# Optimization experiments

Measured on AMD Instinct MI355X. Metric: run time of the kernel, lower is better.

The kernel has to match this reference:

```python
import jax, jax.numpy as jnp
import numpy as np

B, T, D, H, O = 128, 1024, 256, 512, 256


def setup_inputs() -> dict:
    key = jax.random.key(0)
    ks = jax.random.split(key, 7)
    s = lambda k, shape, fan: jax.random.normal(k, shape, dtype=jnp.float32) / np.sqrt(fan)
    return {
        "x": jax.random.normal(ks[0], (B, T, D), dtype=jnp.float32),
        "W_ih": s(ks[1], (4 * H, D), D),
        "W_hh": s(ks[2], (4 * H, H), H),
        "b_ih": jnp.zeros((4 * H,), dtype=jnp.float32),
        "b_hh": jnp.zeros((4 * H,), dtype=jnp.float32),
        "W_out": s(ks[5], (O, H), H),
        "b_out": jnp.zeros((O,), dtype=jnp.float32),
    }


def reference(x, W_ih, W_hh, b_ih, b_hh, W_out, b_out):
    Bsz = x.shape[0]
    Hd = W_hh.shape[1]
    # Precompute input projections for all timesteps: [B, T, 4H]
    x_proj = jnp.einsum("btd,gd->btg", x, W_ih) + b_ih + b_hh

    def step(carry, xp_t):
        h, c = carry
        gates = xp_t + h @ W_hh.T  # [B, 4H]
        i, f, g, o = jnp.split(gates, 4, axis=-1)
        i = jax.nn.sigmoid(i)
        f = jax.nn.sigmoid(f)
        g = jnp.tanh(g)
        o = jax.nn.sigmoid(o)
        c = f * c + i * g
        h = o * jnp.tanh(c)
        return (h, c), None

    h0 = jnp.zeros((Bsz, Hd), dtype=x.dtype)
    c0 = jnp.zeros((Bsz, Hd), dtype=x.dtype)
    (h_T, _), _ = jax.lax.scan(step, (h0, c0), jnp.swapaxes(x_proj, 0, 1))
    return h_T @ W_out.T + b_out
```

## Files before the change

kernel.cpp:

```cpp
#include <hip/hip_runtime.h>

#define Bsz 128
#define Tlen 1024
#define Din 256
#define Hdim 512

#define NBG 8
#define NCG 16

typedef __attribute__((ext_vector_type(8))) short short8;
typedef __attribute__((ext_vector_type(4))) float f32x4;
typedef __attribute__((ext_vector_type(4))) unsigned short ushort4_;
typedef __attribute__((ext_vector_type(4))) unsigned int uint4v;

#define HBT_BYTES ((size_t)2 * NBG * 16 * Hdim * 4)
#define HT_OFF ((size_t)524288)

__device__ inline unsigned short f2bf(float f) {
    unsigned int u = __builtin_bit_cast(unsigned int, f);
    unsigned int lsb = (u >> 16) & 1u;
    u += 0x7fffu + lsb;
    return (unsigned short)(u >> 16);
}
__device__ inline float bf2f(unsigned short u) {
    unsigned int v = ((unsigned int)u) << 16;
    return __builtin_bit_cast(float, v);
}
__device__ inline float sigm_f(float x) { return 1.f / (1.f + __expf(-x)); }
__device__ inline float tanh_f(float x) { return 1.f - 2.f / (__expf(2.f * x) + 1.f); }

__device__ __forceinline__ void conv_x_to_lds(const float4* xv, int tid,
                                              unsigned char* xh, unsigned char* xl) {
#pragma unroll
    for (int i = 0; i < 2; i++) {
        int cidx = tid + i * 512;
        int row = cidx >> 6;
        int c4 = cidx & 63;
        float vv[4] = {xv[i].x, xv[i].y, xv[i].z, xv[i].w};
        ushort4_ vh, vl;
#pragma unroll
        for (int e = 0; e < 4; e++) {
            unsigned short hi = f2bf(vv[e]);
            vh[e] = hi;
            vl[e] = f2bf(vv[e] - bf2f(hi));
        }
        int a = ((row << 9) + (c4 << 3)) ^ ((row & 7) << 4);
        *(ushort4_*)(xh + a) = vh;
        *(ushort4_*)(xl + a) = vl;
    }
}

__device__ __forceinline__ bool chunk_ok(uint4v v, unsigned want) {
    unsigned m =
        ((v[0] ^ want) | (v[1] ^ want) | (v[2] ^ want) | (v[3] ^ want)) & 0xFFFFu;
    return m == 0;
}
__device__ __forceinline__ void chunk_to_lds(uint4v v, int c, unsigned char* h_lds) {
    int row = c >> 7;
    unsigned lo = (v[0] >> 16) | (v[1] & 0xFFFF0000u);
    unsigned hi = (v[2] >> 16) | (v[3] & 0xFFFF0000u);
    int a = ((row << 10) + ((c & 127) << 3)) ^ ((row & 7) << 4);
    *(unsigned long long*)(h_lds + a) =
        (unsigned long long)lo | ((unsigned long long)hi << 32);
}

__global__ __launch_bounds__(512, 1) void lstm_persist(
    const float* __restrict__ x, const float* __restrict__ Wih,
    const float* __restrict__ Whh, const float* __restrict__ bih,
    const float* __restrict__ bhh, unsigned int* __restrict__ hbt,
    float* __restrict__ hT) {
    __shared__ unsigned char h_lds[16 * 1024];
    __shared__ unsigned char xh_lds[2 * 8192];
    __shared__ unsigned char xl_lds[2 * 8192];
    __shared__ float gates_w[8][16 * 17];

    const int tid = threadIdx.x;
    const int bid = blockIdx.x;
    const int bg = bid & 7;
    const int cg = bid >> 3;
    const int lane = tid & 63;
    const int w = tid >> 6;
    const int n15 = lane & 15;
    const int k8 = lane >> 4;
    const int grow = bg * 16;
    const int gc = n15 & 3;
    const int gsel = n15 >> 2;
    const int myb = k8 * 4 + gsel;
    const int mycol = cg * 32 + w * 4 + gc;

    const int R = (n15 >> 2) * Hdim + mycol;
    short8 whh[16], wihh[8], wihl[8];
    {
        const float* wr = Whh + (size_t)R * Hdim;
#pragma unroll
        for (int kc = 0; kc < 16; kc++) {
            const float* p = wr + kc * 32 + k8 * 8;
            short8 f;
#pragma unroll
            for (int e = 0; e < 8; e++) f[e] = (short)f2bf(p[e]);
            whh[kc] = f;
        }
        const float* wr2 = Wih + (size_t)R * Din;
#pragma unroll
        for (int kc = 0; kc < 8; kc++) {
            const float* p = wr2 + kc * 32 + k8 * 8;
            short8 fh, fl;
#pragma unroll
            for (int e = 0; e < 8; e++) {
                float v = p[e];
                unsigned short hi = f2bf(v);
                fh[e] = (short)hi;
                fl[e] = (short)f2bf(v - bf2f(hi));
            }
            wihh[kc] = fh;
            wihl[kc] = fl;
        }
    }
    float bias4[4];
#pragma unroll
    for (int g = 0; g < 4; g++) bias4[g] = bih[g * Hdim + mycol] + bhh[g * Hdim + mycol];

    float4 xr[2];
    {
        const float* xb = x + (size_t)grow * (Tlen * Din);
#pragma unroll
        for (int i = 0; i < 2; i++) {
            int cidx = tid + i * 512;
            int row = cidx >> 6;
            int c4 = cidx & 63;
            xr[i] = *(const float4*)(xb + (size_t)row * (Tlen * Din) + c4 * 4);
        }
        conv_x_to_lds(xr, tid, xh_lds, xl_lds);
#pragma unroll
        for (int i = 0; i < 2; i++) {
            int cidx = tid + i * 512;
            int row = cidx >> 6;
            int c4 = cidx & 63;
            xr[i] = *(const float4*)(xb + (size_t)row * (Tlen * Din) + Din + c4 * 4);
        }
    }
    __syncthreads();

    float c_reg = 0.f, h_last = 0.f;

    for (int t = 0; t < Tlen; ++t) {
        if (t + 1 < Tlen)
            conv_x_to_lds(xr, tid, xh_lds + ((t + 1) & 1) * 8192,
                          xl_lds + ((t + 1) & 1) * 8192);

        const unsigned int* hb = hbt + ((size_t)(t & 1) * NBG + bg) * 8192;
        const unsigned int* p0 = hb + (size_t)tid * 4;
        const unsigned int* p1 = hb + (size_t)(tid + 512) * 4;
        const unsigned int* p2 = hb + (size_t)(tid + 1024) * 4;
        const unsigned int* p3 = hb + (size_t)(tid + 1536) * 4;
        uint4v r0, r1, r2, r3;
        if (t > 0) {
            asm volatile(
                "global_load_dwordx4 %0, %4, off sc0 sc1\n\t"
                "global_load_dwordx4 %1, %5, off sc0 sc1\n\t"
                "global_load_dwordx4 %2, %6, off sc0 sc1\n\t"
                "global_load_dwordx4 %3, %7, off sc0 sc1"
                : "=&v"(r0), "=&v"(r1), "=&v"(r2), "=&v"(r3)
                : "v"(p0), "v"(p1), "v"(p2), "v"(p3)
                : "memory");
        }

        unsigned char* xh = xh_lds + (t & 1) * 8192;
        unsigned char* xl = xl_lds + (t & 1) * 8192;
        f32x4 acc0 = {0.f, 0.f, 0.f, 0.f}, acc1 = {0.f, 0.f, 0.f, 0.f};
#pragma unroll
        for (int kc = 0; kc < 8; kc++) {
            int a = ((n15 << 9) + (kc << 6) + (k8 << 4)) ^ ((n15 & 7) << 4);
            short8 xhv = *(const short8*)(xh + a);
            short8 xlv = *(const short8*)(xl + a);
            acc0 = __builtin_amdgcn_mfma_f32_16x16x32_bf16(xhv, wihh[kc], acc0, 0, 0, 0);
            acc1 = __builtin_amdgcn_mfma_f32_16x16x32_bf16(xlv, wihh[kc], acc1, 0, 0, 0);
            if (kc & 1)
                acc1 = __builtin_amdgcn_mfma_f32_16x16x32_bf16(xhv, wihl[kc], acc1, 0, 0, 0);
            else
                acc0 = __builtin_amdgcn_mfma_f32_16x16x32_bf16(xhv, wihl[kc], acc0, 0, 0, 0);
        }

        if (t > 0) {
            const unsigned want = (unsigned)t;
            asm volatile("s_waitcnt vmcnt(0)" ::: "memory");
            __builtin_amdgcn_sched_barrier(0);
            unsigned need = 0;
            if (chunk_ok(r0, want)) chunk_to_lds(r0, tid, h_lds); else need |= 1u;
            if (chunk_ok(r1, want)) chunk_to_lds(r1, tid + 512, h_lds); else need |= 2u;
            if (chunk_ok(r2, want)) chunk_to_lds(r2, tid + 1024, h_lds); else need |= 4u;
            if (chunk_ok(r3, want)) chunk_to_lds(r3, tid + 1536, h_lds); else need |= 8u;
            int rounds = 0;
            while (need && ++rounds < (1 << 14)) {
                if (rounds > 6) __builtin_amdgcn_s_sleep(2);
                if (need & 1u)
                    asm volatile("global_load_dwordx4 %0, %1, off sc0 sc1"
                                 : "=&v"(r0) : "v"(p0) : "memory");
                if (need & 2u)
                    asm volatile("global_load_dwordx4 %0, %1, off sc0 sc1"
                                 : "=&v"(r1) : "v"(p1) : "memory");
                if (need & 4u)
                    asm volatile("global_load_dwordx4 %0, %1, off sc0 sc1"
                                 : "=&v"(r2) : "v"(p2) : "memory");
                if (need & 8u)
                    asm volatile("global_load_dwordx4 %0, %1, off sc0 sc1"
                                 : "=&v"(r3) : "v"(p3) : "memory");
                asm volatile("s_waitcnt vmcnt(0)" ::: "memory");
                __builtin_amdgcn_sched_barrier(0);
                if ((need & 1u) && chunk_ok(r0, want)) {
                    chunk_to_lds(r0, tid, h_lds);
                    need &= ~1u;
                }
                if ((need & 2u) && chunk_ok(r1, want)) {
                    chunk_to_lds(r1, tid + 512, h_lds);
                    need &= ~2u;
                }
                if ((need & 4u) && chunk_ok(r2, want)) {
                    chunk_to_lds(r2, tid + 1024, h_lds);
                    need &= ~4u;
                }
                if ((need & 8u) && chunk_ok(r3, want)) {
                    chunk_to_lds(r3, tid + 1536, h_lds);
                    need &= ~8u;
                }
            }
        } else {
#pragma unroll
            for (int i = 0; i < 4; i++) {
                int c = tid + i * 512;
                int row = c >> 7;
                int a = ((row << 10) + ((c & 127) << 3)) ^ ((row & 7) << 4);
                *(unsigned long long*)(h_lds + a) = 0ULL;
            }
        }
        __syncthreads();

#pragma unroll
        for (int kc = 0; kc < 16; kc++) {
            short8 a = *(const short8*)(h_lds + (((n15 << 10) + (kc << 6) + (k8 << 4)) ^
                                                ((n15 & 7) << 4)));
            if (kc & 1)
                acc1 = __builtin_amdgcn_mfma_f32_16x16x32_bf16(a, whh[kc], acc1, 0, 0, 0);
            else
                acc0 = __builtin_amdgcn_mfma_f32_16x16x32_bf16(a, whh[kc], acc0, 0, 0, 0);
        }

        if (t + 2 < Tlen) {
            const float* xb = x + (size_t)grow * (Tlen * Din) + (size_t)(t + 2) * Din;
#pragma unroll
            for (int i = 0; i < 2; i++) {
                int cidx = tid + i * 512;
                int row = cidx >> 6;
                int c4 = cidx & 63;
                xr[i] = *(const float4*)(xb + (size_t)row * (Tlen * Din) + c4 * 4);
            }
        }

        float* gt = gates_w[w];
#pragma unroll
        for (int j2 = 0; j2 < 4; j2++) gt[(k8 * 4 + j2) * 17 + n15] = acc0[j2] + acc1[j2];
        {
            float pre[4];
#pragma unroll
            for (int g = 0; g < 4; g++) pre[g] = gt[myb * 17 + g * 4 + gc] + bias4[g];
            float ig = sigm_f(pre[0]);
            float fg = sigm_f(pre[1]);
            float gg = tanh_f(pre[2]);
            float og = sigm_f(pre[3]);
            c_reg = fg * c_reg + ig * gg;
            h_last = og * tanh_f(c_reg);
            unsigned int word = ((unsigned int)f2bf(h_last) << 16) | (unsigned)(t + 1);
            unsigned int* dst = hbt + ((size_t)((t + 1) & 1) * NBG + bg) * 8192 +
                                (size_t)myb * Hdim + mycol;
            __hip_atomic_store(dst, word, __ATOMIC_RELAXED, __HIP_MEMORY_SCOPE_AGENT);
        }
        __syncthreads();
    }

    hT[(size_t)(grow + myb) * Hdim + mycol] = h_last;
}

__global__ __launch_bounds__(256) void out_proj(const float* __restrict__ hT,
                                                const float* __restrict__ Wout,
                                                const float* __restrict__ bout,
                                                float* __restrict__ out) {
    __shared__ float h_s[16 * 512];
    __shared__ float w_s[64 * 69];
    const int tid = threadIdx.x;
    const int bt = blockIdx.x >> 2;
    const int ot = blockIdx.x & 3;
#pragma unroll
    for (int i = 0; i < 8; i++) {
        int cidx = tid + i * 256;
        int row = cidx >> 7;
        int c4 = cidx & 127;
        *(float4*)(&h_s[row * 512 + c4 * 4]) =
            *(const float4*)(hT + (size_t)(bt * 16 + row) * 512 + c4 * 4);
    }
    const int o = tid & 63;
    const int bq = tid >> 6;
    float acc[4] = {0.f, 0.f, 0.f, 0.f};
    for (int kc = 0; kc < 8; kc++) {
        __syncthreads();
#pragma unroll
        for (int i = 0; i < 4; i++) {
            int cidx = tid + i * 256;
            int row = cidx >> 4;
            int c4 = cidx & 15;
            float4 v = *(const float4*)(Wout + (size_t)(ot * 64 + row) * 512 + kc * 64 +
                                        c4 * 4);
            float* dst = &w_s[row * 69 + c4 * 4];
            dst[0] = v.x;
            dst[1] = v.y;
            dst[2] = v.z;
            dst[3] = v.w;
        }
        __syncthreads();
#pragma unroll 16
        for (int k = 0; k < 64; k++) {
            float wv = w_s[o * 69 + k];
#pragma unroll
            for (int bi = 0; bi < 4; bi++)
                acc[bi] += h_s[(bq * 4 + bi) * 512 + kc * 64 + k] * wv;
        }
    }
    float bo = bout[ot * 64 + o];
#pragma unroll
    for (int bi = 0; bi < 4; bi++)
        out[(size_t)(bt * 16 + bq * 4 + bi) * 256 + ot * 64 + o] = acc[bi] + bo;
}

extern "C" void kernel_launch(void* const* d_in, const int* in_sizes, int n_in,
                              void* d_out, int out_size, void* d_ws, size_t ws_size,
                              hipStream_t stream) {
    const float* x = (const float*)d_in[0];
    const float* Wih = (const float*)d_in[1];
    const float* Whh = (const float*)d_in[2];
    const float* bih = (const float*)d_in[3];
    const float* bhh = (const float*)d_in[4];
    const float* Wout = (const float*)d_in[5];
    const float* bout = (const float*)d_in[6];
    float* out = (float*)d_out;

    char* ws = (char*)d_ws;
    unsigned int* hbt = (unsigned int*)ws;
    float* hT = (float*)(ws + HT_OFF);

    hipMemsetAsync(hbt, 0, HBT_BYTES, stream);
    lstm_persist<<<dim3(NBG * NCG), dim3(512), 0, stream>>>(x, Wih, Whh, bih, bhh, hbt,
                                                            hT);
    out_proj<<<dim3(32), dim3(256), 0, stream>>>(hT, Wout, bout, out);
}
```

Measured before the change: 2.176 ms.

## Split input projection into separate parallel kernel feeding the recurrent loop

Adds a separate kernel that computes the input projection for all timesteps in parallel (split-bf16 MFMA) and writes it to a 1 GiB workspace buffer. The persistent recurrent kernel then only loads the precomputed projection per step and starts its accumulators from it, removing the x conversion and input MFMAs from the serial critical path. This costs a large extra HBM write and read. The old fused kernel is kept as a fallback when the workspace is too small.

Measured after the change: 2.182 ms. About the same (+0.3%).

```diff
diff --git a/kernel.cpp b/kernel.cpp
--- a/kernel.cpp
+++ b/kernel.cpp
@@ -15,6 +15,8 @@
 
 #define HBT_BYTES ((size_t)2 * NBG * 16 * Hdim * 4)
 #define HT_OFF ((size_t)524288)
+#define XP_OFF ((size_t)786432)
+#define XP_BYTES ((size_t)1 << 30)
 
 __device__ inline unsigned short f2bf(float f) {
     unsigned int u = __builtin_bit_cast(unsigned int, f);
@@ -64,16 +66,100 @@
         (unsigned long long)lo | ((unsigned long long)hi << 32);
 }
 
-__global__ __launch_bounds__(512, 1) void lstm_persist(
-    const float* __restrict__ x, const float* __restrict__ Wih,
-    const float* __restrict__ Whh, const float* __restrict__ bih,
-    const float* __restrict__ bhh, unsigned int* __restrict__ hbt,
-    float* __restrict__ hT) {
-    __shared__ unsigned char h_lds[16 * 1024];
+__global__ __launch_bounds__(512, 1) void xproj_kernel(const float* __restrict__ x,
+                                                       const float* __restrict__ Wih,
+                                                       float4* __restrict__ xp) {
     __shared__ unsigned char xh_lds[2 * 8192];
     __shared__ unsigned char xl_lds[2 * 8192];
+    const int tid = threadIdx.x;
+    const int bid = blockIdx.x;
+    const int bg = bid & 7;
+    const int cg = (bid >> 3) & 15;
+    const int half = bid >> 7;
+    const int lane = tid & 63;
+    const int w = tid >> 6;
+    const int n15 = lane & 15;
+    const int k8 = lane >> 4;
+    const int grow = bg * 16;
+    const int gc = n15 & 3;
+    const int mycol = cg * 32 + w * 4 + gc;
+    const int R = (n15 >> 2) * Hdim + mycol;
+
+    short8 wihh[8], wihl[8];
+    {
+        const float* wr2 = Wih + (size_t)R * Din;
+#pragma unroll
+        for (int kc = 0; kc < 8; kc++) {
+            const float* p = wr2 + kc * 32 + k8 * 8;
+            short8 fh, fl;
+#pragma unroll
+            for (int e = 0; e < 8; e++) {
+                float v = p[e];
+                unsigned short hi = f2bf(v);
+                fh[e] = (short)hi;
+                fl[e] = (short)f2bf(v - bf2f(hi));
+            }
+            wihh[kc] = fh;
+            wihl[kc] = fl;
+        }
+    }
+    const int t0 = half * 512, t1 = t0 + 512;
+    float4 xr[2];
+    {
+        const float* xb = x + (size_t)grow * (Tlen * Din) + (size_t)t0 * Din;
+#pragma unroll
+        for (int i = 0; i < 2; i++) {
+            int cidx = tid + i * 512;
+            int row = cidx >> 6;
+            int c4 = cidx & 63;
+            xr[i] = *(const float4*)(xb + (size_t)row * (Tlen * Din) + c4 * 4);
+        }
+    }
+    for (int t = t0; t < t1; ++t) {
+        conv_x_to_lds(xr, tid, xh_lds + (t & 1) * 8192, xl_lds + (t & 1) * 8192);
+        if (t + 1 < t1) {
+            const float* xb = x + (size_t)grow * (Tlen * Din) + (size_t)(t + 1) * Din;
+#pragma unroll
+            for (int i = 0; i < 2; i++) {
+                int cidx = tid + i * 512;
+                int row = cidx >> 6;
+                int c4 = cidx & 63;
+                xr[i] = *(const float4*)(xb + (size_t)row * (Tlen * Din) + c4 * 4);
+            }
+        }
+        asm volatile("s_waitcnt lgkmcnt(0)" ::: "memory");
+        __builtin_amdgcn_s_barrier();
+        __builtin_amdgcn_sched_barrier(0);
+        unsigned char* xh = xh_lds + (t & 1) * 8192;
+        unsigned char* xl = xl_lds + (t & 1) * 8192;
+        f32x4 acc0 = {0.f, 0.f, 0.f, 0.f}, acc1 = {0.f, 0.f, 0.f, 0.f};
+#pragma unroll
+        for (int kc = 0; kc < 8; kc++) {
+            int a = ((n15 << 9) + (kc << 6) + (k8 << 4)) ^ ((n15 & 7) << 4);
+            short8 xhv = *(const short8*)(xh + a);
+            short8 xlv = *(const short8*)(xl + a);
+            acc0 = __builtin_amdgcn_mfma_f32_16x16x32_bf16(xhv, wihh[kc], acc0, 0, 0, 0);
+            acc1 = __builtin_amdgcn_mfma_f32_16x16x32_bf16(xlv, wihh[kc], acc1, 0, 0, 0);
+            if (kc & 1)
+                acc1 = __builtin_amdgcn_mfma_f32_16x16x32_bf16(xhv, wihl[kc], acc1, 0, 0, 0);
+            else
+                acc0 = __builtin_amdgcn_mfma_f32_16x16x32_bf16(xhv, wihl[kc], acc0, 0, 0, 0);
+        }
+        float4 o;
+        o.x = acc0[0] + acc1[0];
+        o.y = acc0[1] + acc1[1];
+        o.z = acc0[2] + acc1[2];
+        o.w = acc0[3] + acc1[3];
+        xp[((size_t)t * 128 + (bg * 16 + cg)) * 512 + tid] = o;
+    }
+}
+
+__global__ __launch_bounds__(512, 1) void lstm_persist_xp(
+    const float4* __restrict__ xp, const float* __restrict__ Whh,
+    const float* __restrict__ bih, const float* __restrict__ bhh,
+    unsigned int* __restrict__ hbt, float* __restrict__ hT) {
+    __shared__ unsigned char h_lds[16 * 1024];
     __shared__ float gates_w[8][16 * 17];
-
     const int tid = threadIdx.x;
     const int bid = blockIdx.x;
     const int bg = bid & 7;
@@ -87,6 +173,149 @@
     const int gsel = n15 >> 2;
     const int myb = k8 * 4 + gsel;
     const int mycol = cg * 32 + w * 4 + gc;
+    const int R = (n15 >> 2) * Hdim + mycol;
+
+    short8 whh[16];
+    {
+        const float* wr = Whh + (size_t)R * Hdim;
+#pragma unroll
+        for (int kc = 0; kc < 16; kc++) {
+            const float* p = wr + kc * 32 + k8 * 8;
+            short8 f;
+#pragma unroll
+            for (int e = 0; e < 8; e++) f[e] = (short)f2bf(p[e]);
+            whh[kc] = f;
+        }
+    }
+    float bias4[4];
+#pragma unroll
+    for (int g = 0; g < 4; g++) bias4[g] = bih[g * Hdim + mycol] + bhh[g * Hdim + mycol];
+
+    const size_t xpbase = (size_t)(bg * 16 + cg) * 512 + tid;
+    float4 xpc = xp[xpbase];
+    float c_reg = 0.f, h_last = 0.f;
+
+    for (int t = 0; t < Tlen; ++t) {
+        const unsigned int* hb = hbt + ((size_t)(t & 1) * NBG + bg) * 8192;
+        const unsigned int* p0 = hb + (size_t)tid * 4;
+        const unsigned int* p1 = hb + (size_t)(tid + 512) * 4;
+        const unsigned int* p2 = hb + (size_t)(tid + 1024) * 4;
+        const unsigned int* p3 = hb + (size_t)(tid + 1536) * 4;
+        if (t > 0) {
+            uint4v r0, r1, r2, r3;
+            asm volatile(
+                "global_load_dwordx4 %0, %4, off sc0 sc1\n\t"
+                "global_load_dwordx4 %1, %5, off sc0 sc1\n\t"
+                "global_load_dwordx4 %2, %6, off sc0 sc1\n\t"
+                "global_load_dwordx4 %3, %7, off sc0 sc1"
+                : "=&v"(r0), "=&v"(r1), "=&v"(r2), "=&v"(r3)
+                : "v"(p0), "v"(p1), "v"(p2), "v"(p3)
+                : "memory");
+            const unsigned want = (unsigned)t;
+            asm volatile("s_waitcnt vmcnt(0)" ::: "memory");
+            __builtin_amdgcn_sched_barrier(0);
+            unsigned need = 0;
+            if (chunk_ok(r0, want)) chunk_to_lds(r0, tid, h_lds); else need |= 1u;
+            if (chunk_ok(r1, want)) chunk_to_lds(r1, tid + 512, h_lds); else need |= 2u;
+            if (chunk_ok(r2, want)) chunk_to_lds(r2, tid + 1024, h_lds); else need |= 4u;
+            if (chunk_ok(r3, want)) chunk_to_lds(r3, tid + 1536, h_lds); else need |= 8u;
+            int rounds = 0;
+            while (need && ++rounds < (1 << 14)) {
+                if (rounds > 6) __builtin_amdgcn_s_sleep(2);
+                if (need & 1u)
+                    asm volatile("global_load_dwordx4 %0, %1, off sc0 sc1"
+                                 : "=&v"(r0) : "v"(p0) : "memory");
+                if (need & 2u)
+                    asm volatile("global_load_dwordx4 %0, %1, off sc0 sc1"
+                                 : "=&v"(r1) : "v"(p1) : "memory");
+                if (need & 4u)
+                    asm volatile("global_load_dwordx4 %0, %1, off sc0 sc1"
+                                 : "=&v"(r2) : "v"(p2) : "memory");
+                if (need & 8u)
+                    asm volatile("global_load_dwordx4 %0, %1, off sc0 sc1"
+                                 : "=&v"(r3) : "v"(p3) : "memory");
+                asm volatile("s_waitcnt vmcnt(0)" ::: "memory");
+                __builtin_amdgcn_sched_barrier(0);
+                if ((need & 1u) && chunk_ok(r0, want)) { chunk_to_lds(r0, tid, h_lds); need &= ~1u; }
+                if ((need & 2u) && chunk_ok(r1, want)) { chunk_to_lds(r1, tid + 512, h_lds); need &= ~2u; }
+                if ((need & 4u) && chunk_ok(r2, want)) { chunk_to_lds(r2, tid + 1024, h_lds); need &= ~4u; }
+                if ((need & 8u) && chunk_ok(r3, want)) { chunk_to_lds(r3, tid + 1536, h_lds); need &= ~8u; }
+            }
+        } else {
+#pragma unroll
+            for (int i = 0; i < 4; i++) {
+                int c = tid + i * 512;
+                int row = c >> 7;
+                int a = ((row << 10) + ((c & 127) << 3)) ^ ((row & 7) << 4);
+                *(unsigned long long*)(h_lds + a) = 0ULL;
+            }
+        }
+        float4 xpn = xpc;
+        if (t + 1 < Tlen) xpn = xp[(size_t)(t + 1) * (128 * 512) + xpbase];
+        asm volatile("s_waitcnt lgkmcnt(0)" ::: "memory");
+        __builtin_amdgcn_s_barrier();
+        __builtin_amdgcn_sched_barrier(0);
+
+        f32x4 acc0 = {xpc.x, xpc.y, xpc.z, xpc.w};
+        f32x4 acc1 = {0.f, 0.f, 0.f, 0.f};
+#pragma unroll
+        for (int kc = 0; kc < 16; kc++) {
+            short8 a = *(const short8*)(h_lds + (((n15 << 10) + (kc << 6) + (k8 << 4)) ^
+                                                ((n15 & 7) << 4)));
+            if (kc & 1)
+                acc1 = __builtin_amdgcn_mfma_f32_16x16x32_bf16(a, whh[kc], acc1, 0, 0, 0);
+            else
+                acc0 = __builtin_amdgcn_mfma_f32_16x16x32_bf16(a, whh[kc], acc0, 0, 0, 0);
+        }
+        float* gt = gates_w[w];
+#pragma unroll
+        for (int j2 = 0; j2 < 4; j2++) gt[(k8 * 4 + j2) * 17 + n15] = acc0[j2] + acc1[j2];
+        {
+            float pre[4];
+#pragma unroll
+            for (int g = 0; g < 4; g++) pre[g] = gt[myb * 17 + g * 4 + gc] + bias4[g];
+            float ig = sigm_f(pre[0]);
+            float fg = sigm_f(pre[1]);
+            float gg = tanh_f(pre[2]);
+            float og = sigm_f(pre[3]);
+            c_reg = fg * c_reg + ig * gg;
+            h_last = og * tanh_f(c_reg);
+            unsigned int word = ((unsigned int)f2bf(h_last) << 16) | (unsigned)(t + 1);
+            unsigned int* dst = hbt + ((size_t)((t + 1) & 1) * NBG + bg) * 8192 +
+                                (size_t)myb * Hdim + mycol;
+            __hip_atomic_store(dst, word, __ATOMIC_RELAXED, __HIP_MEMORY_SCOPE_AGENT);
+        }
+        xpc = xpn;
+        asm volatile("s_waitcnt lgkmcnt(0)" ::: "memory");
+        __builtin_amdgcn_s_barrier();
+        __builtin_amdgcn_sched_barrier(0);
+    }
+    hT[(size_t)(grow + myb) * Hdim + mycol] = h_last;
+}
+
+__global__ __launch_bounds__(512, 1) void lstm_persist_fused(
+    const float* __restrict__ x, const float* __restrict__ Wih,
+    const float* __restrict__ Whh, const float* __restrict__ bih,
+    const float* __restrict__ bhh, unsigned int* __restrict__ hbt,
+    float* __restrict__ hT) {
+    __shared__ unsigned char h_lds[16 * 1024];
+    __shared__ unsigned char xh_lds[2 * 8192];
+    __shared__ unsigned char xl_lds[2 * 8192];
+    __shared__ float gates_w[8][16 * 17];
+
+    const int tid = threadIdx.x;
+    const int bid = blockIdx.x;
+    const int bg = bid & 7;
+    const int cg = bid >> 3;
+    const int lane = tid & 63;
+    const int w = tid >> 6;
+    const int n15 = lane & 15;
+    const int k8 = lane >> 4;
+    const int grow = bg * 16;
+    const int gc = n15 & 3;
+    const int gsel = n15 >> 2;
+    const int myb = k8 * 4 + gsel;
+    const int mycol = cg * 32 + w * 4 + gc;
 
     const int R = (n15 >> 2) * Hdim + mycol;
     short8 whh[16], wihh[8], wihl[8];
@@ -147,7 +376,6 @@
         if (t + 1 < Tlen)
             conv_x_to_lds(xr, tid, xh_lds + ((t + 1) & 1) * 8192,
                           xl_lds + ((t + 1) & 1) * 8192);
-
         const unsigned int* hb = hbt + ((size_t)(t & 1) * NBG + bg) * 8192;
         const unsigned int* p0 = hb + (size_t)tid * 4;
         const unsigned int* p1 = hb + (size_t)(tid + 512) * 4;
@@ -164,7 +392,6 @@
                 : "v"(p0), "v"(p1), "v"(p2), "v"(p3)
                 : "memory");
         }
-
         unsigned char* xh = xh_lds + (t & 1) * 8192;
         unsigned char* xl = xl_lds + (t & 1) * 8192;
         f32x4 acc0 = {0.f, 0.f, 0.f, 0.f}, acc1 = {0.f, 0.f, 0.f, 0.f};
@@ -180,7 +407,6 @@
             else
                 acc0 = __builtin_amdgcn_mfma_f32_16x16x32_bf16(xhv, wihl[kc], acc0, 0, 0, 0);
         }
-
         if (t > 0) {
             const unsigned want = (unsigned)t;
             asm volatile("s_waitcnt vmcnt(0)" ::: "memory");
@@ -207,22 +433,10 @@
                                  : "=&v"(r3) : "v"(p3) : "memory");
                 asm volatile("s_waitcnt vmcnt(0)" ::: "memory");
                 __builtin_amdgcn_sched_barrier(0);
-                if ((need & 1u) && chunk_ok(r0, want)) {
-                    chunk_to_lds(r0, tid, h_lds);
-                    need &= ~1u;
-                }
-                if ((need & 2u) && chunk_ok(r1, want)) {
-                    chunk_to_lds(r1, tid + 512, h_lds);
-                    need &= ~2u;
-                }
-                if ((need & 4u) && chunk_ok(r2, want)) {
-                    chunk_to_lds(r2, tid + 1024, h_lds);
-                    need &= ~4u;
-                }
-                if ((need & 8u) && chunk_ok(r3, want)) {
-                    chunk_to_lds(r3, tid + 1536, h_lds);
-                    need &= ~8u;
-                }
+                if ((need & 1u) && chunk_ok(r0, want)) { chunk_to_lds(r0, tid, h_lds); need &= ~1u; }
+                if ((need & 2u) && chunk_ok(r1, want)) { chunk_to_lds(r1, tid + 512, h_lds); need &= ~2u; }
+                if ((need & 4u) && chunk_ok(r2, want)) { chunk_to_lds(r2, tid + 1024, h_lds); need &= ~4u; }
+                if ((need & 8u) && chunk_ok(r3, want)) { chunk_to_lds(r3, tid + 1536, h_lds); need &= ~8u; }
             }
         } else {
 #pragma unroll
@@ -234,7 +448,6 @@
             }
         }
         __syncthreads();
-
 #pragma unroll
         for (int kc = 0; kc < 16; kc++) {
             short8 a = *(const short8*)(h_lds + (((n15 << 10) + (kc << 6) + (k8 << 4)) ^
@@ -244,7 +457,6 @@
             else
                 acc0 = __builtin_amdgcn_mfma_f32_16x16x32_bf16(a, whh[kc], acc0, 0, 0, 0);
         }
-
         if (t + 2 < Tlen) {
             const float* xb = x + (size_t)grow * (Tlen * Din) + (size_t)(t + 2) * Din;
 #pragma unroll
@@ -255,7 +467,6 @@
                 xr[i] = *(const float4*)(xb + (size_t)row * (Tlen * Din) + c4 * 4);
             }
         }
-
         float* gt = gates_w[w];
 #pragma unroll
         for (int j2 = 0; j2 < 4; j2++) gt[(k8 * 4 + j2) * 17 + n15] = acc0[j2] + acc1[j2];
@@ -276,7 +487,6 @@
         }
         __syncthreads();
     }
-
     hT[(size_t)(grow + myb) * Hdim + mycol] = h_last;
 }
 
@@ -345,9 +555,16 @@
     char* ws = (char*)d_ws;
     unsigned int* hbt = (unsigned int*)ws;
     float* hT = (float*)(ws + HT_OFF);
+    float4* xp = (float4*)(ws + XP_OFF);
 
     hipMemsetAsync(hbt, 0, HBT_BYTES, stream);
-    lstm_persist<<<dim3(NBG * NCG), dim3(512), 0, stream>>>(x, Wih, Whh, bih, bhh, hbt,
-                                                            hT);
+    if (ws_size >= XP_OFF + XP_BYTES) {
+        xproj_kernel<<<dim3(256), dim3(512), 0, stream>>>(x, Wih, xp);
+        lstm_persist_xp<<<dim3(NBG * NCG), dim3(512), 0, stream>>>(xp, Whh, bih, bhh,
+                                                                   hbt, hT);
+    } else {
+        lstm_persist_fused<<<dim3(NBG * NCG), dim3(512), 0, stream>>>(x, Wih, Whh, bih,
+                                                                      bhh, hbt, hT);
+    }
     out_proj<<<dim3(32), dim3(256), 0, stream>>>(hT, Wout, bout, out);
 }
```

## Drop split-bf16 input projection, preconvert x to bf16 in a separate pass

Applied to the files above, without the earlier changes.

Removes the hi/lo bf16 split of x and W_ih, so the input projection uses one bf16 MFMA per chunk instead of three. A new xconv kernel converts all of x to bf16 in workspace beforehand, which halves per-step global loads and removes per-step conversion work inside the recurrence. The input-projection MFMAs now run before the h polling loads are issued, __syncthreads is replaced by an explicit lgkmcnt wait plus s_barrier, and the spin sleep is shortened. Accuracy drops because the input projection loses its compensated precision, and the extra conversion pass adds memory traffic.

Result: faster. 2.011 ms (median of 2 runs) (-7.6%).

```diff
diff --git a/kernel.cpp b/kernel.cpp
--- a/kernel.cpp
+++ b/kernel.cpp
@@ -15,6 +15,8 @@
 
 #define HBT_BYTES ((size_t)2 * NBG * 16 * Hdim * 4)
 #define HT_OFF ((size_t)524288)
+#define XB_OFF ((size_t)786432)
+#define XB_BYTES ((size_t)Bsz * Tlen * Din * 2)
 
 __device__ inline unsigned short f2bf(float f) {
     unsigned int u = __builtin_bit_cast(unsigned int, f);
@@ -22,33 +24,8 @@
     u += 0x7fffu + lsb;
     return (unsigned short)(u >> 16);
 }
-__device__ inline float bf2f(unsigned short u) {
-    unsigned int v = ((unsigned int)u) << 16;
-    return __builtin_bit_cast(float, v);
-}
 __device__ inline float sigm_f(float x) { return 1.f / (1.f + __expf(-x)); }
 __device__ inline float tanh_f(float x) { return 1.f - 2.f / (__expf(2.f * x) + 1.f); }
-
-__device__ __forceinline__ void conv_x_to_lds(const float4* xv, int tid,
-                                              unsigned char* xh, unsigned char* xl) {
-#pragma unroll
-    for (int i = 0; i < 2; i++) {
-        int cidx = tid + i * 512;
-        int row = cidx >> 6;
-        int c4 = cidx & 63;
-        float vv[4] = {xv[i].x, xv[i].y, xv[i].z, xv[i].w};
-        ushort4_ vh, vl;
-#pragma unroll
-        for (int e = 0; e < 4; e++) {
-            unsigned short hi = f2bf(vv[e]);
-            vh[e] = hi;
-            vl[e] = f2bf(vv[e] - bf2f(hi));
-        }
-        int a = ((row << 9) + (c4 << 3)) ^ ((row & 7) << 4);
-        *(ushort4_*)(xh + a) = vh;
-        *(ushort4_*)(xl + a) = vl;
-    }
-}
 
 __device__ __forceinline__ bool chunk_ok(uint4v v, unsigned want) {
     unsigned m =
@@ -64,14 +41,32 @@
         (unsigned long long)lo | ((unsigned long long)hi << 32);
 }
 
-__global__ __launch_bounds__(512, 1) void lstm_persist(
-    const float* __restrict__ x, const float* __restrict__ Wih,
-    const float* __restrict__ Whh, const float* __restrict__ bih,
-    const float* __restrict__ bhh, unsigned int* __restrict__ hbt,
-    float* __restrict__ hT) {
+__global__ __launch_bounds__(256) void xconv(const float* __restrict__ x,
+                                             unsigned short* __restrict__ xb) {
+    const size_t nthreads = (size_t)2048 * 256;
+#pragma unroll
+    for (int it = 0; it < 8; ++it) {
+        size_t base =
+            ((size_t)blockIdx.x * 256 + threadIdx.x + it * nthreads) * 8;
+        float4 a = *(const float4*)(x + base);
+        float4 b = *(const float4*)(x + base + 4);
+        short8 o;
+        o[0] = (short)f2bf(a.x); o[1] = (short)f2bf(a.y);
+        o[2] = (short)f2bf(a.z); o[3] = (short)f2bf(a.w);
+        o[4] = (short)f2bf(b.x); o[5] = (short)f2bf(b.y);
+        o[6] = (short)f2bf(b.z); o[7] = (short)f2bf(b.w);
+        *(short8*)(xb + base) = o;
+    }
+}
+
+template <bool XB>
+__global__ __launch_bounds__(512, 1) void lstm_persist_t(
+    const float* __restrict__ x, const unsigned short* __restrict__ xb,
+    const float* __restrict__ Wih, const float* __restrict__ Whh,
+    const float* __restrict__ bih, const float* __restrict__ bhh,
+    unsigned int* __restrict__ hbt, float* __restrict__ hT) {
     __shared__ unsigned char h_lds[16 * 1024];
     __shared__ unsigned char xh_lds[2 * 8192];
-    __shared__ unsigned char xl_lds[2 * 8192];
     __shared__ float gates_w[8][16 * 17];
 
     const int tid = threadIdx.x;
@@ -87,9 +82,9 @@
     const int gsel = n15 >> 2;
     const int myb = k8 * 4 + gsel;
     const int mycol = cg * 32 + w * 4 + gc;
-
     const int R = (n15 >> 2) * Hdim + mycol;
-    short8 whh[16], wihh[8], wihl[8];
+
+    short8 whh[16], wihh[8];
     {
         const float* wr = Whh + (size_t)R * Hdim;
 #pragma unroll
@@ -104,39 +99,46 @@
 #pragma unroll
         for (int kc = 0; kc < 8; kc++) {
             const float* p = wr2 + kc * 32 + k8 * 8;
-            short8 fh, fl;
-#pragma unroll
-            for (int e = 0; e < 8; e++) {
-                float v = p[e];
-                unsigned short hi = f2bf(v);
-                fh[e] = (short)hi;
-                fl[e] = (short)f2bf(v - bf2f(hi));
-            }
-            wihh[kc] = fh;
-            wihl[kc] = fl;
+            short8 f;
+#pragma unroll
+            for (int e = 0; e < 8; e++) f[e] = (short)f2bf(p[e]);
+            wihh[kc] = f;
         }
     }
     float bias4[4];
 #pragma unroll
     for (int g = 0; g < 4; g++) bias4[g] = bih[g * Hdim + mycol] + bhh[g * Hdim + mycol];
 
-    float4 xr[2];
-    {
-        const float* xb = x + (size_t)grow * (Tlen * Din);
+    const int xrow = XB ? (tid >> 5) : 0;
+    const int xc8 = XB ? (tid & 31) : 0;
+    short8 xr8;
+    float4 xrf[2];
+
+    if (XB) {
+        const unsigned short* xrowp = xb + ((size_t)(grow + xrow) * Tlen) * Din;
+        short8 v = *(const short8*)(xrowp + (size_t)0 * Din + xc8 * 8);
+        int a = ((xrow << 9) + (xc8 << 4)) ^ ((xrow & 7) << 4);
+        *(short8*)(xh_lds + a) = v;
+        xr8 = *(const short8*)(xrowp + (size_t)1 * Din + xc8 * 8);
+    } else {
+        const float* xbase = x + (size_t)grow * (Tlen * Din);
 #pragma unroll
         for (int i = 0; i < 2; i++) {
             int cidx = tid + i * 512;
             int row = cidx >> 6;
             int c4 = cidx & 63;
-            xr[i] = *(const float4*)(xb + (size_t)row * (Tlen * Din) + c4 * 4);
-        }
-        conv_x_to_lds(xr, tid, xh_lds, xl_lds);
+            float4 v = *(const float4*)(xbase + (size_t)row * (Tlen * Din) + c4 * 4);
+            ushort4_ vh;
+            vh[0] = f2bf(v.x); vh[1] = f2bf(v.y); vh[2] = f2bf(v.z); vh[3] = f2bf(v.w);
+            int a = ((row << 9) + (c4 << 3)) ^ ((row & 7) << 4);
+            *(ushort4_*)(xh_lds + a) = vh;
+        }
 #pragma unroll
         for (int i = 0; i < 2; i++) {
             int cidx = tid + i * 512;
             int row = cidx >> 6;
             int c4 = cidx & 63;
-            xr[i] = *(const float4*)(xb + (size_t)row * (Tlen * Din) + Din + c4 * 4);
+            xrf[i] = *(const float4*)(xbase + (size_t)row * (Tlen * Din) + Din + c4 * 4);
         }
     }
     __syncthreads();
@@ -144,17 +146,45 @@
     float c_reg = 0.f, h_last = 0.f;
 
     for (int t = 0; t < Tlen; ++t) {
-        if (t + 1 < Tlen)
-            conv_x_to_lds(xr, tid, xh_lds + ((t + 1) & 1) * 8192,
-                          xl_lds + ((t + 1) & 1) * 8192);
-
-        const unsigned int* hb = hbt + ((size_t)(t & 1) * NBG + bg) * 8192;
-        const unsigned int* p0 = hb + (size_t)tid * 4;
-        const unsigned int* p1 = hb + (size_t)(tid + 512) * 4;
-        const unsigned int* p2 = hb + (size_t)(tid + 1024) * 4;
-        const unsigned int* p3 = hb + (size_t)(tid + 1536) * 4;
-        uint4v r0, r1, r2, r3;
+        if (t + 1 < Tlen) {
+            unsigned char* xdst = xh_lds + ((t + 1) & 1) * 8192;
+            if (XB) {
+                int a = ((xrow << 9) + (xc8 << 4)) ^ ((xrow & 7) << 4);
+                *(short8*)(xdst + a) = xr8;
+            } else {
+#pragma unroll
+                for (int i = 0; i < 2; i++) {
+                    int cidx = tid + i * 512;
+                    int row = cidx >> 6;
+                    int c4 = cidx & 63;
+                    ushort4_ vh;
+                    vh[0] = f2bf(xrf[i].x); vh[1] = f2bf(xrf[i].y);
+                    vh[2] = f2bf(xrf[i].z); vh[3] = f2bf(xrf[i].w);
+                    int a = ((row << 9) + (c4 << 3)) ^ ((row & 7) << 4);
+                    *(ushort4_*)(xdst + a) = vh;
+                }
+            }
+        }
+
+        unsigned char* xh = xh_lds + (t & 1) * 8192;
+        f32x4 acc0 = {0.f, 0.f, 0.f, 0.f}, acc1 = {0.f, 0.f, 0.f, 0.f};
+#pragma unroll
+        for (int kc = 0; kc < 8; kc++) {
+            int a = (((n15 << 9) + (kc << 6) + (k8 << 4)) ^ ((n15 & 7) << 4));
+            short8 xv = *(const short8*)(xh + a);
+            if (kc & 1)
+                acc1 = __builtin_amdgcn_mfma_f32_16x16x32_bf16(xv, wihh[kc], acc1, 0, 0, 0);
+            else
+                acc0 = __builtin_amdgcn_mfma_f32_16x16x32_bf16(xv, wihh[kc], acc0, 0, 0, 0);
+        }
+
         if (t > 0) {
+            const unsigned int* hb = hbt + ((size_t)(t & 1) * NBG + bg) * 8192;
+            const unsigned int* p0 = hb + (size_t)tid * 4;
+            const unsigned int* p1 = hb + (size_t)(tid + 512) * 4;
+            const unsigned int* p2 = hb + (size_t)(tid + 1024) * 4;
+            const unsigned int* p3 = hb + (size_t)(tid + 1536) * 4;
+            uint4v r0, r1, r2, r3;
             asm volatile(
                 "global_load_dwordx4 %0, %4, off sc0 sc1\n\t"
                 "global_load_dwordx4 %1, %5, off sc0 sc1\n\t"
@@ -163,25 +193,6 @@
                 : "=&v"(r0), "=&v"(r1), "=&v"(r2), "=&v"(r3)
                 : "v"(p0), "v"(p1), "v"(p2), "v"(p3)
                 : "memory");
-        }
-
-        unsigned char* xh = xh_lds + (t & 1) * 8192;
-        unsigned char* xl = xl_lds + (t & 1) * 8192;
-        f32x4 acc0 = {0.f, 0.f, 0.f, 0.f}, acc1 = {0.f, 0.f, 0.f, 0.f};
-#pragma unroll
-        for (int kc = 0; kc < 8; kc++) {
-            int a = ((n15 << 9) + (kc << 6) + (k8 << 4)) ^ ((n15 & 7) << 4);
-            short8 xhv = *(const short8*)(xh + a);
-            short8 xlv = *(const short8*)(xl + a);
-            acc0 = __builtin_amdgcn_mfma_f32_16x16x32_bf16(xhv, wihh[kc], acc0, 0, 0, 0);
-            acc1 = __builtin_amdgcn_mfma_f32_16x16x32_bf16(xlv, wihh[kc], acc1, 0, 0, 0);
-            if (kc & 1)
-                acc1 = __builtin_amdgcn_mfma_f32_16x16x32_bf16(xhv, wihl[kc], acc1, 0, 0, 0);
-            else
-                acc0 = __builtin_amdgcn_mfma_f32_16x16x32_bf16(xhv, wihl[kc], acc0, 0, 0, 0);
-        }
-
-        if (t > 0) {
             const unsigned want = (unsigned)t;
             asm volatile("s_waitcnt vmcnt(0)" ::: "memory");
             __builtin_amdgcn_sched_barrier(0);
@@ -192,7 +203,7 @@
             if (chunk_ok(r3, want)) chunk_to_lds(r3, tid + 1536, h_lds); else need |= 8u;
             int rounds = 0;
             while (need && ++rounds < (1 << 14)) {
-                if (rounds > 6) __builtin_amdgcn_s_sleep(2);
+                if (rounds > 6) __builtin_amdgcn_s_sleep(1);
                 if (need & 1u)
                     asm volatile("global_load_dwordx4 %0, %1, off sc0 sc1"
                                  : "=&v"(r0) : "v"(p0) : "memory");
@@ -207,22 +218,10 @@
                                  : "=&v"(r3) : "v"(p3) : "memory");
                 asm volatile("s_waitcnt vmcnt(0)" ::: "memory");
                 __builtin_amdgcn_sched_barrier(0);
-                if ((need & 1u) && chunk_ok(r0, want)) {
-                    chunk_to_lds(r0, tid, h_lds);
-                    need &= ~1u;
-                }
-                if ((need & 2u) && chunk_ok(r1, want)) {
-                    chunk_to_lds(r1, tid + 512, h_lds);
-                    need &= ~2u;
-                }
-                if ((need & 4u) && chunk_ok(r2, want)) {
-                    chunk_to_lds(r2, tid + 1024, h_lds);
-                    need &= ~4u;
-                }
-                if ((need & 8u) && chunk_ok(r3, want)) {
-                    chunk_to_lds(r3, tid + 1536, h_lds);
-                    need &= ~8u;
-                }
+                if ((need & 1u) && chunk_ok(r0, want)) { chunk_to_lds(r0, tid, h_lds); need &= ~1u; }
+                if ((need & 2u) && chunk_ok(r1, want)) { chunk_to_lds(r1, tid + 512, h_lds); need &= ~2u; }
+                if ((need & 4u) && chunk_ok(r2, want)) { chunk_to_lds(r2, tid + 1024, h_lds); need &= ~4u; }
+                if ((need & 8u) && chunk_ok(r3, want)) { chunk_to_lds(r3, tid + 1536, h_lds); need &= ~8u; }
             }
         } else {
 #pragma unroll
@@ -233,7 +232,9 @@
                 *(unsigned long long*)(h_lds + a) = 0ULL;
             }
         }
-        __syncthreads();
+        asm volatile("s_waitcnt lgkmcnt(0)" ::: "memory");
+        __builtin_amdgcn_s_barrier();
+        __builtin_amdgcn_sched_barrier(0);
 
 #pragma unroll
         for (int kc = 0; kc < 16; kc++) {
@@ -246,13 +247,19 @@
         }
 
         if (t + 2 < Tlen) {
-            const float* xb = x + (size_t)grow * (Tlen * Din) + (size_t)(t + 2) * Din;
-#pragma unroll
-            for (int i = 0; i < 2; i++) {
-                int cidx = tid + i * 512;
-                int row = cidx >> 6;
-                int c4 = cidx & 63;
-                xr[i] = *(const float4*)(xb + (size_t)row * (Tlen * Din) + c4 * 4);
+            if (XB) {
+                xr8 = *(const short8*)(xb + ((size_t)(grow + xrow) * Tlen + (t + 2)) * Din +
+                                       xc8 * 8);
+            } else {
+                const float* xbase =
+                    x + (size_t)grow * (Tlen * Din) + (size_t)(t + 2) * Din;
+#pragma unroll
+                for (int i = 0; i < 2; i++) {
+                    int cidx = tid + i * 512;
+                    int row = cidx >> 6;
+                    int c4 = cidx & 63;
+                    xrf[i] = *(const float4*)(xbase + (size_t)row * (Tlen * Din) + c4 * 4);
+                }
             }
         }
 
@@ -274,9 +281,10 @@
                                 (size_t)myb * Hdim + mycol;
             __hip_atomic_store(dst, word, __ATOMIC_RELAXED, __HIP_MEMORY_SCOPE_AGENT);
         }
-        __syncthreads();
-    }
-
+        asm volatile("s_waitcnt lgkmcnt(0)" ::: "memory");
+        __builtin_amdgcn_s_barrier();
+        __builtin_amdgcn_sched_barrier(0);
+    }
     hT[(size_t)(grow + myb) * Hdim + mycol] = h_last;
 }
 
@@ -345,9 +353,16 @@
     char* ws = (char*)d_ws;
     unsigned int* hbt = (unsigned int*)ws;
     float* hT = (float*)(ws + HT_OFF);
+    unsigned short* xbuf = (unsigned short*)(ws + XB_OFF);
 
     hipMemsetAsync(hbt, 0, HBT_BYTES, stream);
-    lstm_persist<<<dim3(NBG * NCG), dim3(512), 0, stream>>>(x, Wih, Whh, bih, bhh, hbt,
-                                                            hT);
+    if (ws_size >= XB_OFF + XB_BYTES) {
+        xconv<<<dim3(2048), dim3(256), 0, stream>>>(x, xbuf);
+        lstm_persist_t<true><<<dim3(NBG * NCG), dim3(512), 0, stream>>>(
+            x, xbuf, Wih, Whh, bih, bhh, hbt, hT);
+    } else {
+        lstm_persist_t<false><<<dim3(NBG * NCG), dim3(512), 0, stream>>>(
+            x, (const unsigned short*)nullptr, Wih, Whh, bih, bhh, hbt, hT);
+    }
     out_proj<<<dim3(32), dim3(256), 0, stream>>>(hT, Wout, bout, out);
 }
```
